# Kernel tuning notes

Measured on AMD Instinct MI355X. Metric: run time of the kernel, lower is better.

The kernel has to match this reference:

```python
import jax, jax.numpy as jnp
import numpy as np

B, S, E = 2, 4096, 512

def setup_inputs() -> dict:
    key = jax.random.key(0)
    kx, kq, kk, kv, ko = jax.random.split(key, 5)
    scale = 1.0 / np.sqrt(E)  # init-style scaling for weights
    return {
        "x": jax.random.normal(kx, (B, S, E), dtype=jnp.float32),
        "Wq": jax.random.normal(kq, (E, E), dtype=jnp.float32) * scale,
        "Wk": jax.random.normal(kk, (E, E), dtype=jnp.float32) * scale,
        "Wv": jax.random.normal(kv, (E, E), dtype=jnp.float32) * scale,
        "Wo": jax.random.normal(ko, (E, E), dtype=jnp.float32) * scale,
        "bo": jnp.zeros((E,), dtype=jnp.float32),
    }

def reference(x, Wq, Wk, Wv, Wo, bo):
    # nn.Linear: y = x @ W.T  (weights stored [out, in])
    q = jnp.einsum("bse,fe->bsf", x, Wq)
    k = jnp.einsum("bse,fe->bsf", x, Wk)
    v = jnp.einsum("bse,fe->bsf", x, Wv)
    inv_scale = 1.0 / jnp.sqrt(jnp.asarray(x.shape[-1], x.dtype))
    scores = jnp.einsum("bqe,bke->bqk", q, k) * inv_scale  # [B,S,S]
    S_len = x.shape[1]
    # torch.triu(ones) keeps j >= i; masked_fill where triu==0 masks j < i
    row = jnp.arange(S_len)[:, None]
    col = jnp.arange(S_len)[None, :]
    keep = col >= row  # [S,S], faithfully anti-causal as in the source
    scores = jnp.where(keep[None, :, :], scores, jnp.asarray(-jnp.inf, scores.dtype))
    attn = jax.nn.softmax(scores, axis=-1)
    # dropout p=0.0 -> identity
    out = jnp.einsum("bqk,bke->bqe", attn, v)
    return jnp.einsum("bse,fe->bsf", out, Wo) + bo
```

## Files before the change

kernel.cpp:

```cpp
#include <hip/hip_runtime.h>
#include <hip/hip_bf16.h>

#define S_LEN 4096
#define E_DIM 512
#define B_DIM 2
#define M_ROWS (B_DIM * S_LEN)

typedef __attribute__((ext_vector_type(8))) short short8;
typedef __attribute__((ext_vector_type(4))) float floatx4;

__device__ __forceinline__ unsigned short f2bf(float f) {
    unsigned u = __float_as_uint(f);
    unsigned r = (u + 0x7fffu + ((u >> 16) & 1u)) >> 16;
    return (unsigned short)r;
}
__device__ __forceinline__ float bf2f(unsigned short u) {
    return __uint_as_float((unsigned)u << 16);
}

__device__ __forceinline__ void async_copy16(unsigned short* lds, const unsigned short* g) {
    auto gp = (const __attribute__((address_space(1))) unsigned int*)g;
    auto lp = (__attribute__((address_space(3))) unsigned int*)lds;
    __builtin_amdgcn_global_load_lds(gp, lp, 16, 0, 0);
}

struct MapArg { unsigned short m[576]; };

__global__ __launch_bounds__(256) void convert_bf16(
    const float* __restrict__ x,  const float* __restrict__ wq,
    const float* __restrict__ wk, const float* __restrict__ wv,
    const float* __restrict__ wo, unsigned short* __restrict__ dstU,
    unsigned short* __restrict__ dstWo)
{
    long i = (long)blockIdx.x * 1024 + (long)threadIdx.x * 4;
    const float* src; long off; unsigned short* dst; long doff;
    if      (i < 4194304) { src = x;  off = i;           dst = dstU;  doff = i; }
    else if (i < 4456448) { src = wq; off = i - 4194304; dst = dstU;  doff = i; }
    else if (i < 4718592) { src = wk; off = i - 4456448; dst = dstU;  doff = i; }
    else if (i < 4980736) { src = wv; off = i - 4718592; dst = dstU;  doff = i; }
    else                  { src = wo; off = i - 4980736; dst = dstWo; doff = i - 4980736; }
    float4 v = *(const float4*)(src + off);
    ushort4 o;
    o.x = f2bf(v.x); o.y = f2bf(v.y); o.z = f2bf(v.z); o.w = f2bf(v.w);
    *(ushort4*)(dst + doff) = o;
}

__device__ __forceinline__ void gemm_core(
    const unsigned short* __restrict__ A, const unsigned short* __restrict__ W,
    void* __restrict__ Cv, const float* __restrict__ bias, int mode,
    int m0, int n0)
{
    __shared__ unsigned short As[128 * 64];
    __shared__ unsigned short Bs[128 * 64];
    const int tid = threadIdx.x;
    const int lane = tid & 63, wave = tid >> 6;
    const int wm = wave >> 1, wn = wave & 1;
    const int q4 = lane >> 4, l16 = lane & 15;
    const int er = l16 & 7;

    floatx4 acc[4][4];
#pragma unroll
    for (int i = 0; i < 4; ++i)
#pragma unroll
        for (int j = 0; j < 4; ++j) acc[i][j] = (floatx4){0.f, 0.f, 0.f, 0.f};

    const int srow = lane >> 3;
    const int scol = ((lane & 7) ^ srow) << 3;

    for (int k0 = 0; k0 < 512; k0 += 64) {
#pragma unroll
        for (int c = 0; c < 4; ++c) {
            const int rbase = c * 32 + wave * 8;
            async_copy16(&As[rbase * 64],
                         A + (size_t)(m0 + rbase + srow) * 512 + k0 + scol);
            async_copy16(&Bs[rbase * 64],
                         W + (size_t)(n0 + rbase + srow) * 512 + k0 + scol);
        }
        __syncthreads();
        short8 af[4][2], bfr[4][2];
        const int c0 = (q4 ^ er) * 8;
#pragma unroll
        for (int i = 0; i < 4; ++i) {
            const int ra = (wm * 64 + i * 16 + l16) * 64;
            const int rb = (wn * 64 + i * 16 + l16) * 64;
            af[i][0]  = *(const short8*)&As[ra + c0];
            af[i][1]  = *(const short8*)&As[ra + (c0 ^ 32)];
            bfr[i][0] = *(const short8*)&Bs[rb + c0];
            bfr[i][1] = *(const short8*)&Bs[rb + (c0 ^ 32)];
        }
#pragma unroll
        for (int h = 0; h < 2; ++h)
#pragma unroll
            for (int i = 0; i < 4; ++i)
#pragma unroll
                for (int j = 0; j < 4; ++j)
                    acc[i][j] = __builtin_amdgcn_mfma_f32_16x16x32_bf16(
                        af[i][h], bfr[j][h], acc[i][j], 0, 0, 0);
        __syncthreads();
    }

    if (mode == 0) {
        unsigned short* C = (unsigned short*)Cv;
#pragma unroll
        for (int i = 0; i < 4; ++i) {
            int rowb = m0 + wm * 64 + i * 16 + q4 * 4;
#pragma unroll
            for (int j = 0; j < 4; ++j) {
                int col = n0 + wn * 64 + j * 16 + l16;
#pragma unroll
                for (int rg = 0; rg < 4; ++rg)
                    C[(size_t)(rowb + rg) * 512 + col] = f2bf(acc[i][j][rg]);
            }
        }
    } else if (mode == 1) {
        unsigned short* C = (unsigned short*)Cv;
#pragma unroll
        for (int i = 0; i < 4; ++i) {
            int grow = m0 + wm * 64 + i * 16 + q4 * 4;
            int b = grow >> 12, s = grow & 4095;
#pragma unroll
            for (int j = 0; j < 4; ++j) {
                int e = n0 + wn * 64 + j * 16 + l16;
                ushort4 pk;
                pk.x = f2bf(acc[i][j][0]); pk.y = f2bf(acc[i][j][1]);
                pk.z = f2bf(acc[i][j][2]); pk.w = f2bf(acc[i][j][3]);
                *(ushort4*)(C + (size_t)b * 512 * 4096 + (size_t)e * 4096 + s) = pk;
            }
        }
    } else {
        float* C = (float*)Cv;
#pragma unroll
        for (int i = 0; i < 4; ++i) {
            int rowb = m0 + wm * 64 + i * 16 + q4 * 4;
#pragma unroll
            for (int j = 0; j < 4; ++j) {
                int col = n0 + wn * 64 + j * 16 + l16;
                float bv = bias[col];
#pragma unroll
                for (int rg = 0; rg < 4; ++rg)
                    C[(size_t)(rowb + rg) * 512 + col] = acc[i][j][rg] + bv;
            }
        }
    }
}

__global__ __launch_bounds__(256) void gemm_qkv(
    const unsigned short* __restrict__ xb,
    const unsigned short* __restrict__ Wqb, const unsigned short* __restrict__ Wkb,
    const unsigned short* __restrict__ Wvb,
    unsigned short* __restrict__ Qb, unsigned short* __restrict__ Kb,
    unsigned short* __restrict__ Vtb)
{
    const int z = blockIdx.z;
    const unsigned short* W = (z == 0) ? Wqb : (z == 1) ? Wkb : Wvb;
    unsigned short* C = (z == 0) ? Qb : (z == 1) ? Kb : Vtb;
    gemm_core(xb, W, C, nullptr, (z == 2) ? 1 : 0, blockIdx.y * 128, blockIdx.x * 128);
}

__global__ __launch_bounds__(256) void gemm_out(
    const unsigned short* __restrict__ AOb, const unsigned short* __restrict__ Wob,
    const float* __restrict__ bo, float* __restrict__ out)
{
    gemm_core(AOb, Wob, out, bo, 2, blockIdx.y * 128, blockIdx.x * 128);
}

__global__ __launch_bounds__(512, 2) void flash_mfma(
    const unsigned short* __restrict__ Qg, const unsigned short* __restrict__ Kg,
    const unsigned short* __restrict__ Vt,
    unsigned short* __restrict__ Oh, float* __restrict__ Lb, MapArg map)
{
    const int enc = map.m[blockIdx.x];
    const int tile = enc & 63, ch = (enc >> 6) & 7, bb = enc >> 9;
    const int i0 = tile * 64;
    const int lo0 = 512 * ch, hi = lo0 + 512;
    const int lo = (i0 > lo0) ? i0 : lo0;
    const int lo_al = lo & ~127;
    const int nsteps = (hi - lo_al) >> 7;

    const int tid = threadIdx.x;
    const int lane = tid & 63, w = tid >> 6;
    const int q4 = lane >> 4, l16 = lane & 15;
    const int e = l16 & 7;
    const float scale = 0.044194173824159216f;
    const float MREF = 4.0f;

    __shared__ unsigned short Qs[64 * 512];
    __shared__ unsigned short Plds[2][64][136];
    __shared__ float Lred[8][64];

    const size_t rowbase = (size_t)bb * S_LEN;
    const size_t vbase   = (size_t)bb * (size_t)512 * 4096;

#pragma unroll
    for (int rr = 0; rr < 8; ++rr) {
        const int row = w * 8 + rr;
        const unsigned short* src = Qg + (rowbase + i0 + row) * 512
                                    + ((lane ^ (row & 7)) << 3);
        async_copy16(&Qs[row * 512], src);
    }

    floatx4 oacc[4][4];
#pragma unroll
    for (int mg = 0; mg < 4; ++mg)
#pragma unroll
        for (int nc = 0; nc < 4; ++nc) oacc[mg][nc] = (floatx4){0.f, 0.f, 0.f, 0.f};
    float l_acc[4] = {0.f, 0.f, 0.f, 0.f};

    const unsigned short* qb0 = &Qs[l16 * 512 + ((q4 ^ e) << 3)];
    const unsigned short* qb1 = &Qs[l16 * 512 + (((q4 + 4) ^ e) << 3)];
    const unsigned short* kpbase = Kg + (rowbase + 16 * w + l16) * 512 + (q4 << 3);

    __syncthreads();

    for (int t = 0; t < nsteps; ++t) {
        const int j0 = lo_al + t * 128;
        const int buf = t & 1;

        short8 kf[16];
        const unsigned short* kp = kpbase + (size_t)j0 * 512;
#pragma unroll
        for (int ks = 0; ks < 16; ++ks)
            kf[ks] = *(const short8*)(kp + ks * 32);

        floatx4 sf[4];
#pragma unroll
        for (int mg = 0; mg < 4; ++mg) sf[mg] = (floatx4){0.f, 0.f, 0.f, 0.f};
#pragma unroll
        for (int ks = 0; ks < 16; ++ks) {
            const unsigned short* qb = (ks & 1) ? qb1 : qb0;
#pragma unroll
            for (int mg = 0; mg < 4; ++mg) {
                short8 a = *(const short8*)(qb + mg * 8192 + (ks >> 1) * 64);
                sf[mg] = __builtin_amdgcn_mfma_f32_16x16x32_bf16(kf[ks], a, sf[mg], 0, 0, 0);
            }
        }

        short8 vf[4][4];
#pragma unroll
        for (int nc = 0; nc < 4; ++nc) {
            const unsigned short* vpn = Vt + vbase
                + (size_t)(w * 64 + nc * 16 + l16) * 4096 + j0 + (q4 << 3);
#pragma unroll
            for (int kslot = 0; kslot < 4; ++kslot)
                vf[nc][kslot] = *(const short8*)(vpn + kslot * 32);
        }

        const int kb = j0 + 16 * w + (q4 << 2);
        const bool full = (j0 >= i0 + 64);
#pragma unroll
        for (int mg = 0; mg < 4; ++mg) {
            const int row = i0 + mg * 16 + l16;
            float p0 = __expf(sf[mg][0] * scale - MREF);
            float p1 = __expf(sf[mg][1] * scale - MREF);
            float p2 = __expf(sf[mg][2] * scale - MREF);
            float p3 = __expf(sf[mg][3] * scale - MREF);
            if (!full) {
                p0 = (kb + 0 >= row) ? p0 : 0.f;
                p1 = (kb + 1 >= row) ? p1 : 0.f;
                p2 = (kb + 2 >= row) ? p2 : 0.f;
                p3 = (kb + 3 >= row) ? p3 : 0.f;
            }
            l_acc[mg] += p0 + p1 + p2 + p3;
            ushort4 pk;
            pk.x = f2bf(p0); pk.y = f2bf(p1); pk.z = f2bf(p2); pk.w = f2bf(p3);
            *(ushort4*)&Plds[buf][mg * 16 + l16][16 * w + (q4 << 2)] = pk;
        }
        __syncthreads();

#pragma unroll
        for (int kslot = 0; kslot < 4; ++kslot) {
#pragma unroll
            for (int mg = 0; mg < 4; ++mg) {
                short8 ap = *(const short8*)&Plds[buf][mg * 16 + l16][kslot * 32 + (q4 << 3)];
#pragma unroll
                for (int nc = 0; nc < 4; ++nc)
                    oacc[mg][nc] = __builtin_amdgcn_mfma_f32_16x16x32_bf16(
                        ap, vf[nc][kslot], oacc[mg][nc], 0, 0, 0);
            }
        }
    }

#pragma unroll
    for (int mg = 0; mg < 4; ++mg) {
        float v = l_acc[mg];
        v += __shfl_xor(v, 16, 64);
        v += __shfl_xor(v, 32, 64);
        if (q4 == 0) Lred[w][mg * 16 + l16] = v;
    }
    __syncthreads();

    const int slot = 8 * ch * (ch + 1) + bb * 8 * (ch + 1) + tile;
    if (tid < 64) {
        float sum = 0.f;
#pragma unroll
        for (int ww = 0; ww < 8; ++ww) sum += Lred[ww][tid];
        Lb[(size_t)slot * 64 + tid] = sum;
    }

    unsigned short* Op = Oh + (size_t)slot * 64 * 512;
#pragma unroll
    for (int mg = 0; mg < 4; ++mg)
#pragma unroll
        for (int nc = 0; nc < 4; ++nc)
#pragma unroll
            for (int rg = 0; rg < 4; ++rg)
                Op[(size_t)(mg * 16 + q4 * 4 + rg) * 512 + w * 64 + nc * 16 + l16]
                    = f2bf(oacc[mg][nc][rg]);
}

__global__ __launch_bounds__(256) void flash_merge(
    const unsigned short* __restrict__ Oh, const float* __restrict__ Lb,
    unsigned short* __restrict__ AO)
{
    const int row = blockIdx.x * 4 + (threadIdx.x >> 6);
    const int c0 = (threadIdx.x & 63) * 8;
    const int bb = row >> 12, i = row & 4095;
    const int t = i >> 6, ri = i & 63;
    const int chmin = i >> 9;
    float lsum = 0.f;
    float v[8] = {0.f, 0.f, 0.f, 0.f, 0.f, 0.f, 0.f, 0.f};
    for (int ch = chmin; ch < 8; ++ch) {
        int slot = 8 * ch * (ch + 1) + bb * 8 * (ch + 1) + t;
        lsum += Lb[(size_t)slot * 64 + ri];
        short8 p = *(const short8*)(Oh + (size_t)slot * 64 * 512
                                    + (size_t)ri * 512 + c0);
#pragma unroll
        for (int k = 0; k < 8; ++k) v[k] += bf2f((unsigned short)p[k]);
    }
    float inv = 1.f / lsum;
    short8 o;
#pragma unroll
    for (int k = 0; k < 8; ++k) o[k] = (short)f2bf(v[k] * inv);
    *(short8*)(AO + (size_t)row * 512 + c0) = o;
}

static MapArg build_map() {
    MapArg mp{};
    for (int x = 0; x < 8; ++x) {
        const int bb = x >> 2;
        const int chs[2] = {7 - (x & 3), x & 3};
        int enc[72], st[72], n = 0;
        for (int ci = 0; ci < 2; ++ci) {
            const int ch = chs[ci];
            for (int t = 0; t < 8 * (ch + 1); ++t) {
                int i0 = t * 64, lo0 = 512 * ch, hi = lo0 + 512;
                int lo = (i0 > lo0) ? i0 : lo0;
                int lo_al = lo & ~127;
                enc[n] = t | (ch << 6) | (bb << 9);
                st[n] = (hi - lo_al) >> 7;
                ++n;
            }
        }
        for (int i = 1; i < n; ++i) {
            int ev = enc[i], sv = st[i], j = i - 1;
            while (j >= 0 && st[j] < sv) { st[j + 1] = st[j]; enc[j + 1] = enc[j]; --j; }
            st[j + 1] = sv; enc[j + 1] = ev;
        }
        for (int j = 0; j < n; ++j) mp.m[x + 8 * j] = (unsigned short)enc[j];
    }
    return mp;
}

extern "C" void kernel_launch(void* const* d_in, const int* in_sizes, int n_in,
                              void* d_out, int out_size, void* d_ws, size_t ws_size,
                              hipStream_t stream) {
    (void)in_sizes; (void)n_in; (void)out_size; (void)ws_size;
    const float* x  = (const float*)d_in[0];
    const float* Wq = (const float*)d_in[1];
    const float* Wk = (const float*)d_in[2];
    const float* Wv = (const float*)d_in[3];
    const float* Wo = (const float*)d_in[4];
    const float* bo = (const float*)d_in[5];
    float* out = (float*)d_out;

    unsigned short* ws  = (unsigned short*)d_ws;
    unsigned short* Wob = ws;
    unsigned short* QAb = ws + 262144;
    unsigned short* Kb  = QAb + 4194304;
    unsigned short* Vtb = Kb + 4194304;
    unsigned short* U   = Vtb + 4194304;
    unsigned short* xb  = U;
    unsigned short* Wqb = U + 4194304;
    unsigned short* Wkb = Wqb + 262144;
    unsigned short* Wvb = Wkb + 262144;
    unsigned short* Ohb = U;
    float* Lbf = (float*)(U + 18874368);

    static const MapArg mp = build_map();

    convert_bf16<<<5120, 256, 0, stream>>>(x, Wq, Wk, Wv, Wo, U, Wob);

    gemm_qkv<<<dim3(4, 64, 3), 256, 0, stream>>>(xb, Wqb, Wkb, Wvb, QAb, Kb, Vtb);

    flash_mfma<<<576, 512, 0, stream>>>(QAb, Kb, Vtb, Ohb, Lbf, mp);

    flash_merge<<<2048, 256, 0, stream>>>(Ohb, Lbf, QAb);

    gemm_out<<<dim3(4, 64), 256, 0, stream>>>(QAb, Wob, bo, out);
}
```

Baseline: 214.9 us.

## Fuse flash partial merge into output projection GEMM A-tile loading

Removes the separate merge kernel: the output GEMM now sums the bf16 partial attention outputs per chunk and normalizes them by the summed softmax denominators while staging its A tile into LDS. This drops one launch and the round trip of the merged activation through global memory. In exchange, each of the four column blocks re-reads all partial chunks for its rows, and these loads sit synchronously inside the k-loop.

```diff
diff --git a/kernel.cpp b/kernel.cpp
--- a/kernel.cpp
+++ b/kernel.cpp
@@ -47,8 +47,7 @@
 
 __device__ __forceinline__ void gemm_core(
     const unsigned short* __restrict__ A, const unsigned short* __restrict__ W,
-    void* __restrict__ Cv, const float* __restrict__ bias, int mode,
-    int m0, int n0)
+    void* __restrict__ Cv, int mode, int m0, int n0)
 {
     __shared__ unsigned short As[128 * 64];
     __shared__ unsigned short Bs[128 * 64];
@@ -112,7 +111,7 @@
                     C[(size_t)(rowb + rg) * 512 + col] = f2bf(acc[i][j][rg]);
             }
         }
-    } else if (mode == 1) {
+    } else {
         unsigned short* C = (unsigned short*)Cv;
 #pragma unroll
         for (int i = 0; i < 4; ++i) {
@@ -125,20 +124,6 @@
                 pk.x = f2bf(acc[i][j][0]); pk.y = f2bf(acc[i][j][1]);
                 pk.z = f2bf(acc[i][j][2]); pk.w = f2bf(acc[i][j][3]);
                 *(ushort4*)(C + (size_t)b * 512 * 4096 + (size_t)e * 4096 + s) = pk;
-            }
-        }
-    } else {
-        float* C = (float*)Cv;
-#pragma unroll
-        for (int i = 0; i < 4; ++i) {
-            int rowb = m0 + wm * 64 + i * 16 + q4 * 4;
-#pragma unroll
-            for (int j = 0; j < 4; ++j) {
-                int col = n0 + wn * 64 + j * 16 + l16;
-                float bv = bias[col];
-#pragma unroll
-                for (int rg = 0; rg < 4; ++rg)
-                    C[(size_t)(rowb + rg) * 512 + col] = acc[i][j][rg] + bv;
             }
         }
     }
@@ -154,14 +139,125 @@
     const int z = blockIdx.z;
     const unsigned short* W = (z == 0) ? Wqb : (z == 1) ? Wkb : Wvb;
     unsigned short* C = (z == 0) ? Qb : (z == 1) ? Kb : Vtb;
-    gemm_core(xb, W, C, nullptr, (z == 2) ? 1 : 0, blockIdx.y * 128, blockIdx.x * 128);
-}
-
-__global__ __launch_bounds__(256) void gemm_out(
-    const unsigned short* __restrict__ AOb, const unsigned short* __restrict__ Wob,
-    const float* __restrict__ bo, float* __restrict__ out)
+    gemm_core(xb, W, C, (z == 2) ? 1 : 0, blockIdx.y * 128, blockIdx.x * 128);
+}
+
+__global__ __launch_bounds__(256) void gemm_out_fused(
+    const unsigned short* __restrict__ Oh, const float* __restrict__ Lb,
+    const unsigned short* __restrict__ Wob, const float* __restrict__ bo,
+    float* __restrict__ out)
 {
-    gemm_core(AOb, Wob, out, bo, 2, blockIdx.y * 128, blockIdx.x * 128);
+    __shared__ unsigned short As[128 * 64];
+    __shared__ unsigned short Bs[128 * 64];
+    __shared__ float linv[128];
+    const int tid = threadIdx.x;
+    const int lane = tid & 63, wave = tid >> 6;
+    const int wm = wave >> 1, wn = wave & 1;
+    const int q4 = lane >> 4, l16 = lane & 15;
+    const int er = l16 & 7;
+    const int m0 = blockIdx.y * 128, n0 = blockIdx.x * 128;
+
+    if (tid < 128) {
+        const int grow = m0 + tid;
+        const int bb = grow >> 12, i = grow & 4095;
+        const int t = i >> 6, ri = i & 63, chmin = i >> 9;
+        float ls = 0.f;
+        for (int ch = chmin; ch < 8; ++ch) {
+            int slot = 8 * ch * (ch + 1) + bb * 8 * (ch + 1) + t;
+            ls += Lb[(size_t)slot * 64 + ri];
+        }
+        linv[tid] = 1.f / ls;
+    }
+
+    const int mr = tid >> 1;
+    const int half = tid & 1;
+    const int growM = m0 + mr;
+    const int bbM = growM >> 12, iM = growM & 4095;
+    const int tM = iM >> 6, riM = iM & 63, chminM = iM >> 9;
+
+    const int srow = lane >> 3;
+    const int scol = ((lane & 7) ^ srow) << 3;
+
+    floatx4 acc[4][4];
+#pragma unroll
+    for (int i = 0; i < 4; ++i)
+#pragma unroll
+        for (int j = 0; j < 4; ++j) acc[i][j] = (floatx4){0.f, 0.f, 0.f, 0.f};
+
+    __syncthreads();
+    const float li = linv[mr];
+
+    for (int k0 = 0; k0 < 512; k0 += 64) {
+#pragma unroll
+        for (int c = 0; c < 4; ++c) {
+            const int rbase = c * 32 + wave * 8;
+            async_copy16(&Bs[rbase * 64],
+                         Wob + (size_t)(n0 + rbase + srow) * 512 + k0 + scol);
+        }
+
+        float va[32];
+#pragma unroll
+        for (int k = 0; k < 32; ++k) va[k] = 0.f;
+        for (int ch = chminM; ch < 8; ++ch) {
+            const int slot = 8 * ch * (ch + 1) + bbM * 8 * (ch + 1) + tM;
+            const unsigned short* p = Oh + ((size_t)slot * 64 + riM) * 512
+                                      + k0 + half * 32;
+#pragma unroll
+            for (int j = 0; j < 4; ++j) {
+                short8 v = *(const short8*)(p + j * 8);
+#pragma unroll
+                for (int k = 0; k < 8; ++k)
+                    va[j * 8 + k] += bf2f((unsigned short)v[k]);
+            }
+        }
+#pragma unroll
+        for (int j = 0; j < 4; ++j) {
+            const int lc = half * 4 + j;
+            const int phys = lc ^ (mr & 7);
+            ushort4 lo4, hi4;
+            lo4.x = f2bf(va[j * 8 + 0] * li); lo4.y = f2bf(va[j * 8 + 1] * li);
+            lo4.z = f2bf(va[j * 8 + 2] * li); lo4.w = f2bf(va[j * 8 + 3] * li);
+            hi4.x = f2bf(va[j * 8 + 4] * li); hi4.y = f2bf(va[j * 8 + 5] * li);
+            hi4.z = f2bf(va[j * 8 + 6] * li); hi4.w = f2bf(va[j * 8 + 7] * li);
+            *(ushort4*)&As[mr * 64 + phys * 8]     = lo4;
+            *(ushort4*)&As[mr * 64 + phys * 8 + 4] = hi4;
+        }
+        __syncthreads();
+
+        short8 af[4][2], bfr[4][2];
+        const int c0 = (q4 ^ er) * 8;
+#pragma unroll
+        for (int i = 0; i < 4; ++i) {
+            const int ra = (wm * 64 + i * 16 + l16) * 64;
+            const int rb = (wn * 64 + i * 16 + l16) * 64;
+            af[i][0]  = *(const short8*)&As[ra + c0];
+            af[i][1]  = *(const short8*)&As[ra + (c0 ^ 32)];
+            bfr[i][0] = *(const short8*)&Bs[rb + c0];
+            bfr[i][1] = *(const short8*)&Bs[rb + (c0 ^ 32)];
+        }
+#pragma unroll
+        for (int h = 0; h < 2; ++h)
+#pragma unroll
+            for (int i = 0; i < 4; ++i)
+#pragma unroll
+                for (int j = 0; j < 4; ++j)
+                    acc[i][j] = __builtin_amdgcn_mfma_f32_16x16x32_bf16(
+                        af[i][h], bfr[j][h], acc[i][j], 0, 0, 0);
+        __syncthreads();
+    }
+
+#pragma unroll
+    for (int i = 0; i < 4; ++i) {
+        int rowb = m0 + wm * 64 + i * 16 + q4 * 4;
+#pragma unroll
+        for (int j = 0; j < 4; ++j) {
+            int col = n0 + wn * 64 + j * 16 + l16;
+            float bv = bo[col];
+#pragma unroll
+            for (int rg = 0; rg < 4; ++rg)
+                out[(size_t)(rowb + rg) * 512 + col] = acc[i][j][rg] + bv;
+        }
+    }
 }
 
 __global__ __launch_bounds__(512, 2) void flash_mfma(
@@ -306,32 +402,6 @@
             for (int rg = 0; rg < 4; ++rg)
                 Op[(size_t)(mg * 16 + q4 * 4 + rg) * 512 + w * 64 + nc * 16 + l16]
                     = f2bf(oacc[mg][nc][rg]);
-}
-
-__global__ __launch_bounds__(256) void flash_merge(
-    const unsigned short* __restrict__ Oh, const float* __restrict__ Lb,
-    unsigned short* __restrict__ AO)
-{
-    const int row = blockIdx.x * 4 + (threadIdx.x >> 6);
-    const int c0 = (threadIdx.x & 63) * 8;
-    const int bb = row >> 12, i = row & 4095;
-    const int t = i >> 6, ri = i & 63;
-    const int chmin = i >> 9;
-    float lsum = 0.f;
-    float v[8] = {0.f, 0.f, 0.f, 0.f, 0.f, 0.f, 0.f, 0.f};
-    for (int ch = chmin; ch < 8; ++ch) {
-        int slot = 8 * ch * (ch + 1) + bb * 8 * (ch + 1) + t;
-        lsum += Lb[(size_t)slot * 64 + ri];
-        short8 p = *(const short8*)(Oh + (size_t)slot * 64 * 512
-                                    + (size_t)ri * 512 + c0);
-#pragma unroll
-        for (int k = 0; k < 8; ++k) v[k] += bf2f((unsigned short)p[k]);
-    }
-    float inv = 1.f / lsum;
-    short8 o;
-#pragma unroll
-    for (int k = 0; k < 8; ++k) o[k] = (short)f2bf(v[k] * inv);
-    *(short8*)(AO + (size_t)row * 512 + c0) = o;
 }
 
 static MapArg build_map() {
@@ -375,8 +445,8 @@
 
     unsigned short* ws  = (unsigned short*)d_ws;
     unsigned short* Wob = ws;
-    unsigned short* QAb = ws + 262144;
-    unsigned short* Kb  = QAb + 4194304;
+    unsigned short* Qb  = ws + 262144;
+    unsigned short* Kb  = Qb + 4194304;
     unsigned short* Vtb = Kb + 4194304;
     unsigned short* U   = Vtb + 4194304;
     unsigned short* xb  = U;
@@ -390,11 +460,9 @@
 
     convert_bf16<<<5120, 256, 0, stream>>>(x, Wq, Wk, Wv, Wo, U, Wob);
 
-    gemm_qkv<<<dim3(4, 64, 3), 256, 0, stream>>>(xb, Wqb, Wkb, Wvb, QAb, Kb, Vtb);
-
-    flash_mfma<<<576, 512, 0, stream>>>(QAb, Kb, Vtb, Ohb, Lbf, mp);
-
-    flash_merge<<<2048, 256, 0, stream>>>(Ohb, Lbf, QAb);
-
-    gemm_out<<<dim3(4, 64), 256, 0, stream>>>(QAb, Wob, bo, out);
-}
+    gemm_qkv<<<dim3(4, 64, 3), 256, 0, stream>>>(xb, Wqb, Wkb, Wvb, Qb, Kb, Vtb);
+
+    flash_mfma<<<576, 512, 0, stream>>>(Qb, Kb, Vtb, Ohb, Lbf, mp);
+
+    gemm_out_fused<<<dim3(4, 64), 256, 0, stream>>>(Ohb, Lbf, Wob, bo, out);
+}
```

After: 236.8 us. 1.1x slower.
